# Kernel tuning notes

Measured on AMD Instinct MI355X. Metric: run time of the kernel, lower is better.

## Reference

```python
import jax, jax.numpy as jnp
import numpy as np

B, T, D = 2, 4096, 1024
KQ = 128   # k_query
K = 8      # top_k


def setup_inputs() -> dict:
    key = jax.random.key(0)
    ks = jax.random.split(key, 7)
    x = jax.random.normal(ks[0], (B, T, D), dtype=jnp.float32)
    attention_mask = jnp.ones((B, T), dtype=jnp.float32)
    # Linear params stored as (in, out) so y = x @ W + b
    Wq = jax.random.normal(ks[1], (D, KQ), dtype=jnp.float32) * 0.02
    bq = jnp.zeros((KQ,), dtype=jnp.float32)
    Wk = jax.random.normal(ks[2], (D, KQ), dtype=jnp.float32) * 0.02
    bk = jnp.zeros((KQ,), dtype=jnp.float32)
    Wg = jax.random.normal(ks[3], (D, 1), dtype=jnp.float32) * 0.02
    bg = jnp.zeros((1,), dtype=jnp.float32)
    return {"x": x, "attention_mask": attention_mask,
            "Wq": Wq, "bq": bq, "Wk": Wk, "bk": bk, "Wg": Wg, "bg": bg}


def reference(x, attention_mask, Wq, bq, Wk, bk, Wg, bg):
    # projections
    q = x @ Wq + bq            # [B,T,KQ]
    k = x @ Wk + bk            # [B,T,KQ]
    scale = 1.0 / (KQ ** 0.5)
    sim = jnp.einsum('btc,bsc->bts', q, k) * scale  # [B,T,T]
    # pairwise mask: mask[b,i,j] = am[b,i]*am[b,j]
    pair = attention_mask[:, :, None] * attention_mask[:, None, :]
    sim = jnp.where(pair == 0, jnp.float32(-1e9), sim)
    # per-query gate scales each row of sim
    gates = jax.nn.sigmoid(x @ Wg + bg)[..., 0]     # [B,T]
    sim = sim * gates[:, :, None]
    # top-k over keys; top_k values == gather(sim, topk_indices)
    sim_gathered, topk_indices = jax.lax.top_k(sim, K)  # [B,T,K]
    # gather full D-dim token rows without materializing [B,T,T,D]
    gathered = jax.vmap(lambda xb, ib: xb[ib])(x, topk_indices)  # [B,T,K,D]
    return (gathered, topk_indices, sim_gathered)
```

## Files before the change

### kernel.cpp

```cpp
#include <hip/hip_runtime.h>
#include <math.h>

#define BB   2
#define TT   4096
#define NT   (BB*TT)
#define DD   1024
#define CQ   128
#define TK   8
#define NCH  16

typedef __attribute__((ext_vector_type(8))) short short8b;
typedef __attribute__((ext_vector_type(4))) float f32x4;

__device__ __forceinline__ void topk8_insert_strict(float (&v)[TK], int (&ix)[TK],
                                                    float val, int idx) {
    float cv = val; int ci = idx;
#pragma unroll
    for (int i = 0; i < TK; ++i) {
        bool sw = (cv > v[i]);
        float tv = v[i]; int ti = ix[i];
        v[i]  = sw ? cv : tv;  ix[i] = sw ? ci : ti;
        cv    = sw ? tv : cv;  ci    = sw ? ti : ci;
    }
}

__device__ __forceinline__ void topk8_insert(float (&v)[TK], int (&ix)[TK],
                                             float val, int idx) {
    float cv = val; int ci = idx;
#pragma unroll
    for (int i = 0; i < TK; ++i) {
        bool sw = (cv > v[i]) || (cv == v[i] && ci < ix[i]);
        float tv = v[i]; int ti = ix[i];
        v[i]  = sw ? cv : tv;  ix[i] = sw ? ci : ti;
        cv    = sw ? tv : cv;  ci    = sw ? ti : ci;
    }
}

__device__ __forceinline__ unsigned int pack_bf16(float a, float b) {
    unsigned int ua = __float_as_uint(a), ub = __float_as_uint(b);
    return (ua >> 16) | (ub & 0xFFFF0000u);
}

__global__ __launch_bounds__(256) void proj_kernel(
    const float* __restrict__ x,
    const float* __restrict__ Wq, const float* __restrict__ bq,
    const float* __restrict__ Wk, const float* __restrict__ bk,
    float* __restrict__ q, float* __restrict__ k)
{
    int row = blockIdx.x * 256 + threadIdx.x;
    int cc  = blockIdx.y * 16;
    bool isK = cc >= CQ;
    const float* W    = isK ? Wk : Wq;
    const float* bias = isK ? bk : bq;
    int c0 = isK ? cc - CQ : cc;

    float acc[16];
#pragma unroll
    for (int j = 0; j < 16; ++j) acc[j] = 0.f;

    const float* xr = x + (size_t)row * DD;
    for (int d0 = 0; d0 < DD; d0 += 4) {
        float4 xv = *reinterpret_cast<const float4*>(xr + d0);
        const float* w0 = W + (size_t)d0 * CQ + c0;
#pragma unroll
        for (int j = 0; j < 16; ++j) {
            acc[j] = fmaf(xv.x, w0[j],        acc[j]);
            acc[j] = fmaf(xv.y, w0[CQ + j],   acc[j]);
            acc[j] = fmaf(xv.z, w0[2*CQ + j], acc[j]);
            acc[j] = fmaf(xv.w, w0[3*CQ + j], acc[j]);
        }
    }
    float* outp = (isK ? k : q) + (size_t)row * CQ + c0;
#pragma unroll
    for (int j = 0; j < 16; ++j) outp[j] = acc[j] + bias[c0 + j];
}

__global__ __launch_bounds__(256) void gate_kernel(
    const float* __restrict__ x, const float* __restrict__ Wg,
    const float* __restrict__ bg, float* __restrict__ gout)
{
    int wave = threadIdx.x >> 6, lane = threadIdx.x & 63;
    int row  = blockIdx.x * 4 + wave;
    const float* xr = x + (size_t)row * DD;
    float s = 0.f;
#pragma unroll
    for (int i = 0; i < 4; ++i) {
        int d = (i * 64 + lane) * 4;
        float4 xv = *reinterpret_cast<const float4*>(xr + d);
        float4 wv = *reinterpret_cast<const float4*>(Wg + d);
        s = fmaf(xv.x, wv.x, s); s = fmaf(xv.y, wv.y, s);
        s = fmaf(xv.z, wv.z, s); s = fmaf(xv.w, wv.w, s);
    }
#pragma unroll
    for (int off = 32; off; off >>= 1) s += __shfl_xor(s, off);
    if (lane == 0) gout[row] = 1.f / (1.f + expf(-(s + bg[0])));
}

__global__ __launch_bounds__(256, 4) void simtopk_kernel(
    const float* __restrict__ qmat, const float* __restrict__ kmat,
    const float* __restrict__ gates, const float* __restrict__ am,
    int* __restrict__ pi)
{
    __shared__ unsigned int Qb[64 * 64];
    __shared__ unsigned int Kb[64 * 64];

    const int tid  = threadIdx.x;
    const int lane = tid & 63;
    const int wv   = tid >> 6;
    const int qt   = blockIdx.x;
    const int sp   = blockIdx.y;
    const int t0   = qt * 64;
    const int b    = t0 >> 12;

    const int sr = tid >> 2;
    const int sg0 = tid & 3;

    {
        const float* src = qmat + (size_t)(t0 + sr) * CQ;
#pragma unroll
        for (int j = 0; j < 4; ++j) {
            int g = sg0 + j * 4;
            float4 f0 = *reinterpret_cast<const float4*>(src + g * 8);
            float4 f1 = *reinterpret_cast<const float4*>(src + g * 8 + 4);
            uint4 u;
            u.x = pack_bf16(f0.x, f0.y); u.y = pack_bf16(f0.z, f0.w);
            u.z = pack_bf16(f1.x, f1.y); u.w = pack_bf16(f1.z, f1.w);
            *reinterpret_cast<uint4*>(&Qb[sr * 64 + ((g ^ (sr & 7)) << 2)]) = u;
        }
    }
    {
        const float* src = kmat + (size_t)(b * TT + sp * 256 + sr) * CQ;
#pragma unroll
        for (int j = 0; j < 4; ++j) {
            int g = sg0 + j * 4;
            float4 f0 = *reinterpret_cast<const float4*>(src + g * 8);
            float4 f1 = *reinterpret_cast<const float4*>(src + g * 8 + 4);
            uint4 u;
            u.x = pack_bf16(f0.x, f0.y); u.y = pack_bf16(f0.z, f0.w);
            u.z = pack_bf16(f1.x, f1.y); u.w = pack_bf16(f1.z, f1.w);
            *reinterpret_cast<uint4*>(&Kb[sr * 64 + ((g ^ (sr & 7)) << 2)]) = u;
        }
    }

    const int l15  = lane & 15;
    const int l4   = lane >> 4;
    const int qrow = wv * 16 + l15;
    const int tq   = t0 + qrow;

    const float gate = gates[tq];
    const float mq   = am[tq];
    const float sgq  = 0.08838834764831845f * gate;
    const float mneg = -1e9f * gate;

    float tv[TK]; int tix[TK];
#pragma unroll
    for (int j = 0; j < TK; ++j) { tv[j] = -3.0e38f; tix[j] = 0; }

    const int koff = l4 * 4;
    __syncthreads();

    for (int ck = 0; ck < 4; ++ck) {
        f32x4 c0 = {0.f, 0.f, 0.f, 0.f};
        f32x4 c1 = {0.f, 0.f, 0.f, 0.f};
        f32x4 c2 = {0.f, 0.f, 0.f, 0.f};
        f32x4 c3 = {0.f, 0.f, 0.f, 0.f};
#pragma unroll
        for (int kb = 0; kb < 4; ++kb) {
            int gq = (kb * 4 + l4);
            short8b bq = *reinterpret_cast<const short8b*>(
                &Qb[qrow * 64 + (((gq) ^ (qrow & 7)) << 2)]);
            int r0 = l15,      p0 = ((gq) ^ (r0 & 7)) << 2;
            int r1 = 16 + l15, p1 = ((gq) ^ (r1 & 7)) << 2;
            int r2 = 32 + l15, p2 = ((gq) ^ (r2 & 7)) << 2;
            int r3 = 48 + l15, p3 = ((gq) ^ (r3 & 7)) << 2;
            short8b a0 = *reinterpret_cast<const short8b*>(&Kb[r0 * 64 + p0]);
            short8b a1 = *reinterpret_cast<const short8b*>(&Kb[r1 * 64 + p1]);
            short8b a2 = *reinterpret_cast<const short8b*>(&Kb[r2 * 64 + p2]);
            short8b a3 = *reinterpret_cast<const short8b*>(&Kb[r3 * 64 + p3]);
            c0 = __builtin_amdgcn_mfma_f32_16x16x32_bf16(a0, bq, c0, 0, 0, 0);
            c1 = __builtin_amdgcn_mfma_f32_16x16x32_bf16(a1, bq, c1, 0, 0, 0);
            c2 = __builtin_amdgcn_mfma_f32_16x16x32_bf16(a2, bq, c2, 0, 0, 0);
            c3 = __builtin_amdgcn_mfma_f32_16x16x32_bf16(a3, bq, c3, 0, 0, 0);
        }

        float4 pf[8];
        if (ck < 3) {
            const float* src = kmat +
                (size_t)(b * TT + sp * 256 + (ck + 1) * 64 + sr) * CQ;
#pragma unroll
            for (int j = 0; j < 4; ++j) {
                int g = sg0 + j * 4;
                pf[j * 2 + 0] = *reinterpret_cast<const float4*>(src + g * 8);
                pf[j * 2 + 1] = *reinterpret_cast<const float4*>(src + g * 8 + 4);
            }
        }

        {
            const int sB = sp * 256 + ck * 64;
            const float* amB = am + b * TT + sB;
            float val;
#define SCAN_TILE(CC, KT)                                                    \
            {                                                                \
                float4 amv = *reinterpret_cast<const float4*>(               \
                    amB + (KT) * 16 + koff);                                 \
                int kbase = sB + (KT) * 16 + koff;                           \
                val = (mq * amv.x == 0.f) ? mneg : CC.x * sgq;               \
                if (val > tv[TK-1]) topk8_insert_strict(tv, tix, val, kbase);\
                val = (mq * amv.y == 0.f) ? mneg : CC.y * sgq;               \
                if (val > tv[TK-1]) topk8_insert_strict(tv, tix, val, kbase+1);\
                val = (mq * amv.z == 0.f) ? mneg : CC.z * sgq;               \
                if (val > tv[TK-1]) topk8_insert_strict(tv, tix, val, kbase+2);\
                val = (mq * amv.w == 0.f) ? mneg : CC.w * sgq;               \
                if (val > tv[TK-1]) topk8_insert_strict(tv, tix, val, kbase+3);\
            }
            SCAN_TILE(c0, 0)
            SCAN_TILE(c1, 1)
            SCAN_TILE(c2, 2)
            SCAN_TILE(c3, 3)
#undef SCAN_TILE
        }
        __syncthreads();

        if (ck < 3) {
#pragma unroll
            for (int j = 0; j < 4; ++j) {
                int g = sg0 + j * 4;
                uint4 u;
                u.x = pack_bf16(pf[j*2].x, pf[j*2].y);
                u.y = pack_bf16(pf[j*2].z, pf[j*2].w);
                u.z = pack_bf16(pf[j*2+1].x, pf[j*2+1].y);
                u.w = pack_bf16(pf[j*2+1].z, pf[j*2+1].w);
                *reinterpret_cast<uint4*>(&Kb[sr * 64 + ((g ^ (sr & 7)) << 2)]) = u;
            }
        }
        __syncthreads();
    }

    float* mv = reinterpret_cast<float*>(Qb);
    int*   mi = reinterpret_cast<int*>(Kb);
    int slot = qrow * 4 + l4;
#pragma unroll
    for (int j = 0; j < TK; ++j) { mv[slot * 9 + j] = tv[j]; mi[slot * 9 + j] = tix[j]; }
    __syncthreads();
    if (l4 == 0) {
        for (int u = 1; u < 4; ++u) {
#pragma unroll
            for (int j = 0; j < TK; ++j) {
                float val = mv[(slot + u) * 9 + j];
                int   s   = mi[(slot + u) * 9 + j];
                if (val > tv[TK-1] || (val == tv[TK-1] && s < tix[TK-1]))
                    topk8_insert(tv, tix, val, s);
            }
        }
        int base = (tq * NCH + sp) * TK;
#pragma unroll
        for (int j = 0; j < TK; ++j) pi[base + j] = tix[j];
    }
}

__global__ __launch_bounds__(256) void merge_gather_kernel(
    const float* __restrict__ x,  const float* __restrict__ qm,
    const float* __restrict__ kmat, const float* __restrict__ gates,
    const float* __restrict__ am, const int* __restrict__ pi,
    float* __restrict__ out_g, float* __restrict__ out_i,
    float* __restrict__ out_v)
{
    int t = blockIdx.x;
    int b = t >> 12;
    int tid = threadIdx.x;

    __shared__ float  qrow[CQ];
    __shared__ double svald[NCH * TK];
    __shared__ int    scand[NCH * TK];
    __shared__ int    fidx[TK];

    if (tid < 32) {
        *reinterpret_cast<float4*>(qrow + tid * 4) =
            *reinterpret_cast<const float4*>(qm + (size_t)t * CQ + tid * 4);
    }
    __syncthreads();

    {
        int c    = tid >> 1;
        int half = tid & 1;
        int s = pi[(size_t)t * NCH * TK + c];
        const float* kr = kmat + (size_t)(b * TT + s) * CQ + half * 64;
        const float* qh = qrow + half * 64;
        double a0 = 0.0, a1 = 0.0, a2 = 0.0, a3 = 0.0;
#pragma unroll
        for (int d = 0; d < 64; d += 4) {
            float4 kv = *reinterpret_cast<const float4*>(kr + d);
            a0 += (double)qh[d + 0] * (double)kv.x;
            a1 += (double)qh[d + 1] * (double)kv.y;
            a2 += (double)qh[d + 2] * (double)kv.z;
            a3 += (double)qh[d + 3] * (double)kv.w;
        }
        double mine  = (a0 + a1) + (a2 + a3);
        double other = __shfl_xor(mine, 1);
        double lo = half ? other : mine;
        double hi = half ? mine  : other;
        double acc = lo + hi;
        if (half == 0) {
            float ms  = am[b * TT + s];
            float mqq = am[t];
            double val = (mqq * ms == 0.f) ? -1e9 : acc * 0.08838834764831845;
            val *= (double)gates[t];
            svald[c] = val;
            scand[c] = s;
        }
    }
    __syncthreads();

    if (tid < NCH * TK) {
        double v = svald[tid]; int si = scand[tid];
        int rank = 0;
        for (int c2 = 0; c2 < NCH * TK; ++c2) {
            double v2 = svald[c2]; int s2 = scand[c2];
            rank += (v2 > v) || (v2 == v && s2 < si);
        }
        if (rank < TK) {
            out_i[t * TK + rank] = (float)si;
            out_v[t * TK + rank] = (float)v;
            fidx[rank] = si;
        }
    }
    __syncthreads();

#pragma unroll
    for (int j = 0; j < TK; ++j) {
        int row = fidx[j];
        float4 val4 = *reinterpret_cast<const float4*>(
            x + ((size_t)(b * TT + row)) * DD + tid * 4);
        *reinterpret_cast<float4*>(
            out_g + ((size_t)(t * TK + j)) * DD + tid * 4) = val4;
    }
}

extern "C" void kernel_launch(void* const* d_in, const int* in_sizes, int n_in,
                              void* d_out, int out_size, void* d_ws, size_t ws_size,
                              hipStream_t stream) {
    const float* x  = (const float*)d_in[0];
    const float* am = (const float*)d_in[1];
    const float* Wq = (const float*)d_in[2];
    const float* bq = (const float*)d_in[3];
    const float* Wk = (const float*)d_in[4];
    const float* bk = (const float*)d_in[5];
    const float* Wg = (const float*)d_in[6];
    const float* bg = (const float*)d_in[7];

    float* ws = (float*)d_ws;
    float* q  = ws;
    float* k  = ws + 1048576;
    float* g  = ws + 2097152;
    int*   pi = (int*)(ws + 2105344);

    float* out_g = (float*)d_out;
    float* out_i = out_g + 67108864;
    float* out_v = out_i + 65536;

    proj_kernel<<<dim3(NT / 256, 16), 256, 0, stream>>>(x, Wq, bq, Wk, bk, q, k);
    gate_kernel<<<NT / 4, 256, 0, stream>>>(x, Wg, bg, g);
    simtopk_kernel<<<dim3(128, NCH), 256, 0, stream>>>(q, k, g, am, pi);
    merge_gather_kernel<<<NT, 256, 0, stream>>>(x, q, k, g, am, pi,
                                                out_g, out_i, out_v);
}
```

Measured before the change: 331.1 us.

## Tile projection GEMM through shared memory and use nontemporal stores for gather output

Rewrites the Q/K projection as a shared-memory tiled GEMM. Each block stages a 64-row by 128-depth slab of x (transposed, padded) and a 128x64 slab of W, and each thread computes a 4x4 register tile. This replaces the old one-row-per-thread loop, which reread each x row 16 times with uncoalesced strided reads. Separately, the 256 MB gather output is now written with nontemporal stores to avoid polluting the cache. The tiled kernel adds LDS usage and barriers, and the grid shrinks to 128x4 blocks.

New measurement: 299.3 us (median of 2 runs). 1.11x faster.

```diff
diff --git a/kernel.cpp b/kernel.cpp
--- a/kernel.cpp
+++ b/kernel.cpp
@@ -47,32 +47,84 @@
     const float* __restrict__ Wk, const float* __restrict__ bk,
     float* __restrict__ q, float* __restrict__ k)
 {
-    int row = blockIdx.x * 256 + threadIdx.x;
-    int cc  = blockIdx.y * 16;
-    bool isK = cc >= CQ;
+    __shared__ float Xs[128 * 68];
+    __shared__ float Ws[128 * 68];
+
+    const int tid = threadIdx.x;
+    const int rg  = tid >> 4;
+    const int cg  = tid & 15;
+    const int r0b = blockIdx.x * 64;
+    const int ccb = blockIdx.y * 64;
+    const bool isK = ccb >= CQ;
     const float* W    = isK ? Wk : Wq;
     const float* bias = isK ? bk : bq;
-    int c0 = isK ? cc - CQ : cc;
+    const int c0b = isK ? ccb - CQ : ccb;
+
+    const int sr = tid >> 2;
+    const int lq = tid & 3;
+    const int wd = tid >> 1;
+    const int wh = tid & 1;
 
     float acc[16];
 #pragma unroll
     for (int j = 0; j < 16; ++j) acc[j] = 0.f;
 
-    const float* xr = x + (size_t)row * DD;
-    for (int d0 = 0; d0 < DD; d0 += 4) {
-        float4 xv = *reinterpret_cast<const float4*>(xr + d0);
-        const float* w0 = W + (size_t)d0 * CQ + c0;
-#pragma unroll
-        for (int j = 0; j < 16; ++j) {
-            acc[j] = fmaf(xv.x, w0[j],        acc[j]);
-            acc[j] = fmaf(xv.y, w0[CQ + j],   acc[j]);
-            acc[j] = fmaf(xv.z, w0[2*CQ + j], acc[j]);
-            acc[j] = fmaf(xv.w, w0[3*CQ + j], acc[j]);
-        }
-    }
-    float* outp = (isK ? k : q) + (size_t)row * CQ + c0;
-#pragma unroll
-    for (int j = 0; j < 16; ++j) outp[j] = acc[j] + bias[c0 + j];
+    for (int dc = 0; dc < DD; dc += 128) {
+#pragma unroll
+        for (int p = 0; p < 8; ++p) {
+            int d = lq * 4 + p * 16;
+            float4 v = *reinterpret_cast<const float4*>(
+                x + (size_t)(r0b + sr) * DD + dc + d);
+            Xs[(d + 0) * 68 + sr] = v.x;
+            Xs[(d + 1) * 68 + sr] = v.y;
+            Xs[(d + 2) * 68 + sr] = v.z;
+            Xs[(d + 3) * 68 + sr] = v.w;
+        }
+#pragma unroll
+        for (int p = 0; p < 8; ++p) {
+            int c = wh * 32 + p * 4;
+            float4 v = *reinterpret_cast<const float4*>(
+                W + (size_t)(dc + wd) * CQ + c0b + c);
+            *reinterpret_cast<float4*>(&Ws[wd * 68 + c]) = v;
+        }
+        __syncthreads();
+
+#pragma unroll 4
+        for (int dd = 0; dd < 128; ++dd) {
+            float4 xv = *reinterpret_cast<const float4*>(&Xs[dd * 68 + rg * 4]);
+            float4 wv = *reinterpret_cast<const float4*>(&Ws[dd * 68 + cg * 4]);
+            acc[0]  = fmaf(xv.x, wv.x, acc[0]);
+            acc[1]  = fmaf(xv.x, wv.y, acc[1]);
+            acc[2]  = fmaf(xv.x, wv.z, acc[2]);
+            acc[3]  = fmaf(xv.x, wv.w, acc[3]);
+            acc[4]  = fmaf(xv.y, wv.x, acc[4]);
+            acc[5]  = fmaf(xv.y, wv.y, acc[5]);
+            acc[6]  = fmaf(xv.y, wv.z, acc[6]);
+            acc[7]  = fmaf(xv.y, wv.w, acc[7]);
+            acc[8]  = fmaf(xv.z, wv.x, acc[8]);
+            acc[9]  = fmaf(xv.z, wv.y, acc[9]);
+            acc[10] = fmaf(xv.z, wv.z, acc[10]);
+            acc[11] = fmaf(xv.z, wv.w, acc[11]);
+            acc[12] = fmaf(xv.w, wv.x, acc[12]);
+            acc[13] = fmaf(xv.w, wv.y, acc[13]);
+            acc[14] = fmaf(xv.w, wv.z, acc[14]);
+            acc[15] = fmaf(xv.w, wv.w, acc[15]);
+        }
+        __syncthreads();
+    }
+
+    float4 bi = *reinterpret_cast<const float4*>(bias + c0b + cg * 4);
+    float* outp = isK ? k : q;
+#pragma unroll
+    for (int i = 0; i < 4; ++i) {
+        float4 o;
+        o.x = acc[i * 4 + 0] + bi.x;
+        o.y = acc[i * 4 + 1] + bi.y;
+        o.z = acc[i * 4 + 2] + bi.z;
+        o.w = acc[i * 4 + 3] + bi.w;
+        *reinterpret_cast<float4*>(
+            outp + (size_t)(r0b + rg * 4 + i) * CQ + c0b + cg * 4) = o;
+    }
 }
 
 __global__ __launch_bounds__(256) void gate_kernel(
@@ -329,10 +381,10 @@
 #pragma unroll
     for (int j = 0; j < TK; ++j) {
         int row = fidx[j];
-        float4 val4 = *reinterpret_cast<const float4*>(
+        f32x4 val4 = *reinterpret_cast<const f32x4*>(
             x + ((size_t)(b * TT + row)) * DD + tid * 4);
-        *reinterpret_cast<float4*>(
-            out_g + ((size_t)(t * TK + j)) * DD + tid * 4) = val4;
+        __builtin_nontemporal_store(val4, reinterpret_cast<f32x4*>(
+            out_g + ((size_t)(t * TK + j)) * DD + tid * 4));
     }
 }
 
@@ -358,7 +410,7 @@
     float* out_i = out_g + 67108864;
     float* out_v = out_i + 65536;
 
-    proj_kernel<<<dim3(NT / 256, 16), 256, 0, stream>>>(x, Wq, bq, Wk, bk, q, k);
+    proj_kernel<<<dim3(NT / 64, 4), 256, 0, stream>>>(x, Wq, bq, Wk, bk, q, k);
     gate_kernel<<<NT / 4, 256, 0, stream>>>(x, Wg, bg, g);
     simtopk_kernel<<<dim3(128, NCH), 256, 0, stream>>>(q, k, g, am, pi);
     merge_gather_kernel<<<NT, 256, 0, stream>>>(x, q, k, g, am, pi,
```
